# Performance work log

Hardware: AMD Instinct MI355X
Metric: run time of the kernel (lower is better)

The kernel has to match this reference:

```python
import jax, jax.numpy as jnp
import numpy as np

# conf[1:] and loss_div_wd[1:] tables from the original module (31 entries each)
CONF = np.float32([0.9991138577461243, 0.8724386692047119, 0.8048540353775024, 0.7398145198822021, 0.6715637445449829, 0.5973713397979736, 0.5154045820236206, 0.42423248291015625, 0.3226756751537323, 0.20976418256759644, 0.08473344892263412, -0.05296758562326431, -0.2036692053079605, -0.3674810528755188, -0.5443023443222046, -0.7338425517082214, -0.9356498718261719, -1.149145483970642, -1.3736592531204224, -1.6084641218185425, -1.8528070449829102, -2.1059343814849854, -2.367111921310425, -2.6356399059295654, -2.910861015319824, -3.1921679973602295, -3.479003667831421, -3.770861864089966, -4.067285060882568, -4.367861747741699, -4.67222261428833])
LOSS_DIV_WD = np.float32([-0.7357585932962737, -0.7292385198866751, -0.7197861042909649, -0.7060825529685993, -0.6862159572880272, -0.6574145455480526, -0.6156599675844636, -0.5551266577364037, -0.46736905653740307, -0.34014329294487, -0.15569892914556094, 0.11169756647530316, 0.4993531412919867, 1.0613531942004133, 1.8761075276533326, 3.0572900212223724, 4.769698321281568, 7.252246278161051, 10.851297017399714, 16.06898724880869, 23.63328498268829, 34.599555050301056, 50.497802769609315, 73.54613907594951, 106.96024960367691, 155.40204460004963, 225.63008495214464, 327.4425312511471, 475.0441754009414, 689.0282819387658, 999.249744])

_LOG = np.log(LOSS_DIV_WD + np.float32(0.750256)).astype(np.float32)
LOG_STEP = np.float32((_LOG[-1] - _LOG[0]) / 2.0)   # step * (N-1) / 2
LOG_OFFSET = np.float32(_LOG[0] + LOG_STEP)
NTAB = CONF.shape[0]  # 31

B, NCLS, NSAMPLES = 32768, 1000, 1000000
SMOOTH_INS = 0.9
SMOOTH_CLS = 0.9
WD_INS = 1.0
WD_CLS = 1.0


def optimal_conf(loss, wd):
    # 1D linear interp emulating F.grid_sample(..., padding_mode='border', align_corners=True)
    l = loss / wd
    ln = (jnp.log(l + 0.750256) - LOG_OFFSET) / LOG_STEP
    ln = jnp.where(jnp.isnan(ln), -1.0, ln)          # NaN (log of negative) -> left border
    ix = jnp.clip((ln + 1.0) * 0.5 * (NTAB - 1), 0.0, NTAB - 1)
    i0 = jnp.floor(ix)
    frac = ix - i0
    i0 = i0.astype(jnp.int32)
    i1 = jnp.minimum(i0 + 1, NTAB - 1)
    tab = jnp.asarray(CONF)
    r = tab[i0] * (1.0 - frac) + tab[i1] * frac
    return jnp.exp(r)


def smoothed(values, idx, memory, smoothing, nseg):
    # EMA smoothing per bin: bincount-with-weights -> per-bin mean -> alpha = smoothing**count
    binned = jax.ops.segment_sum(values, idx, num_segments=nseg)
    cnt = jax.ops.segment_sum(jnp.ones_like(values), idx, num_segments=nseg)
    nnz = cnt > 0
    means = jnp.where(nnz, binned / jnp.maximum(cnt, 1.0), 0.0)
    alpha = smoothing ** cnt
    new_mem = jnp.where(nnz, alpha * memory + (1.0 - alpha) * means, memory)
    return new_mem[idx]


def setup_inputs() -> dict:
    key = jax.random.key(0)
    k1, k2, k3 = jax.random.split(key, 3)
    preds = jax.random.normal(k1, (B, NCLS), dtype=jnp.float32)
    labels = jax.random.randint(k2, (B,), 0, NCLS, dtype=jnp.int32)
    indices = jax.random.randint(k3, (B,), 0, NSAMPLES, dtype=jnp.int32)
    memory_ins = jnp.zeros((NSAMPLES,), dtype=jnp.float32)
    memory_cls = jnp.zeros((NCLS,), dtype=jnp.float32)
    return {"preds": preds, "memory_ins": memory_ins, "memory_cls": memory_cls,
            "labels": labels, "indices": indices}


def reference(preds, memory_ins, memory_cls, labels, indices):
    # per-sample cross entropy (reduction='none')
    logp = jax.nn.log_softmax(preds, axis=-1)
    loss_batch = -jnp.take_along_axis(logp, labels[:, None].astype(jnp.int32), axis=-1)[:, 0]
    lb = jax.lax.stop_gradient(loss_batch)  # loss_batch.detach()
    # instance branch (expectation = Constant(0) -> threshold 0)
    sl_ins = smoothed(lb, indices, memory_ins, SMOOTH_INS, NSAMPLES)
    conf_ins = optimal_conf(sl_ins, WD_INS)
    # class branch
    sl_cls = smoothed(lb, labels, memory_cls, SMOOTH_CLS, NCLS)
    conf_cls = optimal_conf(sl_cls, WD_CLS)
    conf = jax.lax.stop_gradient(conf_ins * conf_cls)
    return (loss_batch * conf).mean()
```

## Files before the change

kernel.cpp:

```cpp
#include <hip/hip_runtime.h>
#include <math.h>

#define B_N 32768
#define NCLS 1000
#define NSAMP 1000000
#define NTAB 31

__constant__ float c_conf[NTAB] = {
    0.9991138577461243f, 0.8724386692047119f, 0.8048540353775024f, 0.7398145198822021f,
    0.6715637445449829f, 0.5973713397979736f, 0.5154045820236206f, 0.42423248291015625f,
    0.3226756751537323f, 0.20976418256759644f, 0.08473344892263412f, -0.05296758562326431f,
    -0.2036692053079605f, -0.3674810528755188f, -0.5443023443222046f, -0.7338425517082214f,
    -0.9356498718261719f, -1.149145483970642f, -1.3736592531204224f, -1.6084641218185425f,
    -1.8528070449829102f, -2.1059343814849854f, -2.367111921310425f, -2.6356399059295654f,
    -2.910861015319824f, -3.1921679973602295f, -3.479003667831421f, -3.770861864089966f,
    -4.067285060882568f, -4.367861747741699f, -4.67222261428833f};

#define LOG_OFFSET 1.3369849f
#define INV_LOG_STEP 0.17950834f
#define LN_SMOOTH -0.10536052f

__device__ __forceinline__ float optimal_conf(float l) {
    float ln = (logf(l + 0.750256f) - LOG_OFFSET) * INV_LOG_STEP;
    if (ln != ln) ln = -1.0f;
    float ix = fminf(fmaxf((ln + 1.0f) * 0.5f * (NTAB - 1), 0.0f), (float)(NTAB - 1));
    float i0f = floorf(ix);
    float frac = ix - i0f;
    int i0 = (int)i0f;
    int i1 = min(i0 + 1, NTAB - 1);
    float r = c_conf[i0] * (1.0f - frac) + c_conf[i1] * frac;
    return expf(r);
}

__global__ __launch_bounds__(256) void ce_loss_kernel(
    const float* __restrict__ preds, const int* __restrict__ labels,
    const int* __restrict__ indices, float* __restrict__ loss,
    float* __restrict__ ins_sum, float* __restrict__ ins_cnt,
    float* __restrict__ cls_sum, float* __restrict__ cls_cnt)
{
    const int row = blockIdx.x;
    const int t = threadIdx.x;
    const float4* p = (const float4*)(preds + (size_t)row * NCLS);

    float4 v = make_float4(-INFINITY, -INFINITY, -INFINITY, -INFINITY);
    if (t < NCLS / 4) v = p[t];

    float m = fmaxf(fmaxf(v.x, v.y), fmaxf(v.z, v.w));
    #pragma unroll
    for (int off = 32; off > 0; off >>= 1) m = fmaxf(m, __shfl_down(m, off, 64));
    __shared__ float sm[4];
    __shared__ float bcast;
    const int wave = t >> 6, lane = t & 63;
    if (lane == 0) sm[wave] = m;
    __syncthreads();
    if (t == 0) bcast = fmaxf(fmaxf(sm[0], sm[1]), fmaxf(sm[2], sm[3]));
    __syncthreads();
    const float M = bcast;

    float s = 0.0f;
    if (t < NCLS / 4)
        s = expf(v.x - M) + expf(v.y - M) + expf(v.z - M) + expf(v.w - M);
    #pragma unroll
    for (int off = 32; off > 0; off >>= 1) s += __shfl_down(s, off, 64);
    __syncthreads();
    if (lane == 0) sm[wave] = s;
    __syncthreads();

    if (t == 0) {
        const float S = sm[0] + sm[1] + sm[2] + sm[3];
        const int lab = labels[row];
        const float l = logf(S) + M - preds[(size_t)row * NCLS + lab];
        loss[row] = l;
        const int idx = indices[row];
        atomicAdd(&ins_sum[idx], l);
        atomicAdd(&ins_cnt[idx], 1.0f);
        atomicAdd(&cls_sum[lab], l);
        atomicAdd(&cls_cnt[lab], 1.0f);
    }
}

__global__ __launch_bounds__(256) void conf_reduce_kernel(
    const float* __restrict__ loss, const int* __restrict__ labels,
    const int* __restrict__ indices,
    const float* __restrict__ mem_ins, const float* __restrict__ mem_cls,
    const float* __restrict__ ins_sum, const float* __restrict__ ins_cnt,
    const float* __restrict__ cls_sum, const float* __restrict__ cls_cnt,
    float* __restrict__ out)
{
    const int i = blockIdx.x * 256 + threadIdx.x;
    float val = 0.0f;
    if (i < B_N) {
        const float l = loss[i];
        const int idx = indices[i];
        const int lab = labels[i];

        const float ci = ins_cnt[idx];
        const float mean_i = ins_sum[idx] / ci;
        const float ai = expf(ci * LN_SMOOTH);
        const float sl_i = ai * mem_ins[idx] + (1.0f - ai) * mean_i;

        const float cc = cls_cnt[lab];
        const float mean_c = cls_sum[lab] / cc;
        const float ac = expf(cc * LN_SMOOTH);
        const float sl_c = ac * mem_cls[lab] + (1.0f - ac) * mean_c;

        const float conf = optimal_conf(sl_i) * optimal_conf(sl_c);
        val = l * conf * (1.0f / (float)B_N);
    }
    #pragma unroll
    for (int off = 32; off > 0; off >>= 1) val += __shfl_down(val, off, 64);
    __shared__ float sm[4];
    const int wave = threadIdx.x >> 6, lane = threadIdx.x & 63;
    if (lane == 0) sm[wave] = val;
    __syncthreads();
    if (threadIdx.x == 0) atomicAdd(out, sm[0] + sm[1] + sm[2] + sm[3]);
}

extern "C" void kernel_launch(void* const* d_in, const int* in_sizes, int n_in,
                              void* d_out, int out_size, void* d_ws, size_t ws_size,
                              hipStream_t stream) {
    const float* preds   = (const float*)d_in[0];
    const float* mem_ins = (const float*)d_in[1];
    const float* mem_cls = (const float*)d_in[2];
    const int*   labels  = (const int*)d_in[3];
    const int*   indices = (const int*)d_in[4];
    float* out = (float*)d_out;

    float* loss    = (float*)d_ws;
    float* ins_sum = loss + B_N;
    float* ins_cnt = ins_sum + NSAMP;
    float* cls_sum = ins_cnt + NSAMP;
    float* cls_cnt = cls_sum + NCLS;

    hipMemsetAsync(ins_sum, 0, (size_t)(2 * NSAMP + 2 * NCLS) * sizeof(float), stream);
    hipMemsetAsync(out, 0, sizeof(float), stream);

    ce_loss_kernel<<<B_N, 256, 0, stream>>>(preds, labels, indices, loss,
                                            ins_sum, ins_cnt, cls_sum, cls_cnt);
    conf_reduce_kernel<<<(B_N + 255) / 256, 256, 0, stream>>>(
        loss, labels, indices, mem_ins, mem_cls,
        ins_sum, ins_cnt, cls_sum, cls_cnt, out);
}
```

Before: 200.3 us.

## Map one wavefront per row in CE kernel and drop output memset

The cross-entropy kernel now processes four rows per 256-thread block, one wavefront per row. Each lane loads up to four float4 values and the reductions use xor shuffles, so block-level shared memory and __syncthreads are no longer needed. The separate memset of the output scalar is removed; block 0 of the first kernel zeroes it instead, which saves one launch. This lowers launch and synchronisation overhead and gives each wave more loads in flight, at the cost of more registers per lane.

New measurement: 203.9 us. No clear change (+1.8%).

```diff
diff --git a/kernel.cpp b/kernel.cpp
--- a/kernel.cpp
+++ b/kernel.cpp
@@ -36,40 +36,41 @@
     const float* __restrict__ preds, const int* __restrict__ labels,
     const int* __restrict__ indices, float* __restrict__ loss,
     float* __restrict__ ins_sum, float* __restrict__ ins_cnt,
-    float* __restrict__ cls_sum, float* __restrict__ cls_cnt)
+    float* __restrict__ cls_sum, float* __restrict__ cls_cnt,
+    float* __restrict__ out)
 {
-    const int row = blockIdx.x;
     const int t = threadIdx.x;
+    const int wave = t >> 6, lane = t & 63;
+    const int row = blockIdx.x * 4 + wave;
+
+    if (blockIdx.x == 0 && t == 0) *out = 0.0f;
+
     const float4* p = (const float4*)(preds + (size_t)row * NCLS);
 
-    float4 v = make_float4(-INFINITY, -INFINITY, -INFINITY, -INFINITY);
-    if (t < NCLS / 4) v = p[t];
+    const float NEG_INF = -INFINITY;
+    float4 v0 = p[lane];
+    float4 v1 = p[lane + 64];
+    float4 v2 = p[lane + 128];
+    float4 v3 = make_float4(NEG_INF, NEG_INF, NEG_INF, NEG_INF);
+    if (lane < 58) v3 = p[lane + 192];
 
-    float m = fmaxf(fmaxf(v.x, v.y), fmaxf(v.z, v.w));
+    float m = fmaxf(fmaxf(fmaxf(v0.x, v0.y), fmaxf(v0.z, v0.w)),
+                    fmaxf(fmaxf(v1.x, v1.y), fmaxf(v1.z, v1.w)));
+    m = fmaxf(m, fmaxf(fmaxf(v2.x, v2.y), fmaxf(v2.z, v2.w)));
+    m = fmaxf(m, fmaxf(fmaxf(v3.x, v3.y), fmaxf(v3.z, v3.w)));
     #pragma unroll
-    for (int off = 32; off > 0; off >>= 1) m = fmaxf(m, __shfl_down(m, off, 64));
-    __shared__ float sm[4];
-    __shared__ float bcast;
-    const int wave = t >> 6, lane = t & 63;
-    if (lane == 0) sm[wave] = m;
-    __syncthreads();
-    if (t == 0) bcast = fmaxf(fmaxf(sm[0], sm[1]), fmaxf(sm[2], sm[3]));
-    __syncthreads();
-    const float M = bcast;
+    for (int off = 32; off > 0; off >>= 1) m = fmaxf(m, __shfl_xor(m, off, 64));
 
-    float s = 0.0f;
-    if (t < NCLS / 4)
-        s = expf(v.x - M) + expf(v.y - M) + expf(v.z - M) + expf(v.w - M);
+    float s = expf(v0.x - m) + expf(v0.y - m) + expf(v0.z - m) + expf(v0.w - m);
+    s += expf(v1.x - m) + expf(v1.y - m) + expf(v1.z - m) + expf(v1.w - m);
+    s += expf(v2.x - m) + expf(v2.y - m) + expf(v2.z - m) + expf(v2.w - m);
+    s += expf(v3.x - m) + expf(v3.y - m) + expf(v3.z - m) + expf(v3.w - m);
     #pragma unroll
-    for (int off = 32; off > 0; off >>= 1) s += __shfl_down(s, off, 64);
-    __syncthreads();
-    if (lane == 0) sm[wave] = s;
-    __syncthreads();
+    for (int off = 32; off > 0; off >>= 1) s += __shfl_xor(s, off, 64);
 
-    if (t == 0) {
-        const float S = sm[0] + sm[1] + sm[2] + sm[3];
+    if (lane == 0) {
         const int lab = labels[row];
-        const float l = logf(S) + M - preds[(size_t)row * NCLS + lab];
+        const float l = logf(s) + m - preds[(size_t)row * NCLS + lab];
         loss[row] = l;
         const int idx = indices[row];
         atomicAdd(&ins_sum[idx], l);
@@ -133,10 +134,9 @@
     float* cls_cnt = cls_sum + NCLS;
 
     hipMemsetAsync(ins_sum, 0, (size_t)(2 * NSAMP + 2 * NCLS) * sizeof(float), stream);
-    hipMemsetAsync(out, 0, sizeof(float), stream);
 
-    ce_loss_kernel<<<B_N, 256, 0, stream>>>(preds, labels, indices, loss,
-                                            ins_sum, ins_cnt, cls_sum, cls_cnt);
+    ce_loss_kernel<<<B_N / 4, 256, 0, stream>>>(preds, labels, indices, loss,
+                                                ins_sum, ins_cnt, cls_sum, cls_cnt, out);
     conf_reduce_kernel<<<(B_N + 255) / 256, 256, 0, stream>>>(
         loss, labels, indices, mem_ins, mem_cls,
         ins_sum, ins_cnt, cls_sum, cls_cnt, out);
```
